# Optimization experiments

Measured on AMD Instinct MI355X. Metric: run time of the kernel, lower is better.

The kernel has to match this reference:

```python
import jax, jax.numpy as jnp
import numpy as np
from jax import lax

SCALE = 0.05  # keep gates out of saturation

def _lstm_layer(x, w_ih, w_hh, b_ih, b_hh):
    # x: [B, T, In]; w_ih: [4H, In]; w_hh: [4H, H]; PyTorch gate order i,f,g,o
    B = x.shape[0]
    H = w_hh.shape[1]
    # precompute input contribution for all timesteps: [B, T, 4H]
    xg = jnp.einsum('bti,gi->btg', x, w_ih) + b_ih + b_hh
    h0 = jnp.zeros((B, H), dtype=x.dtype)
    c0 = jnp.zeros((B, H), dtype=x.dtype)

    def step(carry, xg_t):
        h, c = carry
        gates = xg_t + h @ w_hh.T  # [B, 4H]
        i, f, g, o = jnp.split(gates, 4, axis=-1)
        i = jax.nn.sigmoid(i)
        f = jax.nn.sigmoid(f)
        g = jnp.tanh(g)
        o = jax.nn.sigmoid(o)
        c = f * c + i * g
        h = o * jnp.tanh(c)
        return (h, c), h

    (h_T, c_T), hs = lax.scan(step, (h0, c0), xg.transpose(1, 0, 2))  # hs: [T, B, H]
    return hs.transpose(1, 0, 2), h_T, c_T


def setup_inputs() -> dict:
    key = jax.random.key(0)
    ks = jax.random.split(key, 12)
    B, T, In, H = 128, 1024, 128, 256
    G = 4 * H
    inp = {
        'x': jax.random.normal(ks[0], (B, T, In), dtype=jnp.float32),
        'w_ih_l0': jax.random.normal(ks[1], (G, In), dtype=jnp.float32) * SCALE,
        'w_hh_l0': jax.random.normal(ks[2], (G, H), dtype=jnp.float32) * SCALE,
        'b_ih_l0': jax.random.normal(ks[3], (G,), dtype=jnp.float32) * SCALE,
        'b_hh_l0': jax.random.normal(ks[4], (G,), dtype=jnp.float32) * SCALE,
        'w_ih_l1': jax.random.normal(ks[5], (G, H), dtype=jnp.float32) * SCALE,
        'w_hh_l1': jax.random.normal(ks[6], (G, H), dtype=jnp.float32) * SCALE,
        'b_ih_l1': jax.random.normal(ks[7], (G,), dtype=jnp.float32) * SCALE,
        'b_hh_l1': jax.random.normal(ks[8], (G,), dtype=jnp.float32) * SCALE,
        'w_lin': jax.random.normal(ks[9], (In, H), dtype=jnp.float32) * SCALE,
        'b_lin': jax.random.normal(ks[10], (In,), dtype=jnp.float32) * SCALE,
    }
    return inp


def reference(x, w_ih_l0, w_hh_l0, b_ih_l0, b_hh_l0,
              w_ih_l1, w_hh_l1, b_ih_l1, b_hh_l1, w_lin, b_lin):
    h0_seq, h0, c0 = _lstm_layer(x, w_ih_l0, w_hh_l0, b_ih_l0, b_hh_l0)
    h1_seq, h1, c1 = _lstm_layer(h0_seq, w_ih_l1, w_hh_l1, b_ih_l1, b_hh_l1)
    out = jnp.einsum('bth,oh->bto', h1_seq, w_lin) + b_lin  # [B, T, In]
    h = jnp.stack([h0, h1], axis=0)  # [num_layers, B, H]
    c = jnp.stack([c0, c1], axis=0)
    return out, (h, c)
```

## Files before the change

### kernel.cpp

```cpp
#include <hip/hip_runtime.h>
#include <hip/hip_bf16.h>

typedef __attribute__((ext_vector_type(8))) short short8;
typedef __attribute__((ext_vector_type(4))) float floatx4;
typedef __attribute__((ext_vector_type(4))) unsigned int uint4v;
typedef __attribute__((ext_vector_type(2))) _Float16 f16x2;

#define B_ 128
#define T_ 1024
#define H_ 256
#define G_ 1024

#if defined(__has_builtin)
#  if __has_builtin(__builtin_amdgcn_fdot2)
#    define HAS_FDOT2 1
#  endif
#endif

__device__ __forceinline__ float sigmoidf_(float x) {
    x = fminf(fmaxf(x, -30.f), 30.f);
    return 1.0f / (1.0f + __expf(-x));
}
__device__ __forceinline__ float tanhf_(float x) {
    x = fminf(fmaxf(x, -15.f), 15.f);
    float e = __expf(2.0f * x);
    return 1.0f - 2.0f / (e + 1.0f);
}
__device__ __forceinline__ unsigned short f2bu(float x) {
    __hip_bfloat16 b = __float2bfloat16(x);
    return *reinterpret_cast<unsigned short*>(&b);
}

__device__ __forceinline__ float dot2_(unsigned int w, unsigned int h, float acc) {
#ifdef HAS_FDOT2
    return __builtin_amdgcn_fdot2(__builtin_bit_cast(f16x2, w),
                                  __builtin_bit_cast(f16x2, h), acc, false);
#else
    float d;
    asm("v_dot2_f32_f16 %0, %1, %2, %3" : "=v"(d) : "v"(w), "v"(h), "v"(acc));
    return d;
#endif
}

__global__ __launch_bounds__(256) void gemm_bias_f32(
    const float* __restrict__ A,
    const float* __restrict__ Wt,
    const float* __restrict__ bias1,
    const float* __restrict__ bias2,
    float* __restrict__ C,
    int d2shift, long sa1, long sa2, long sc1, long sc2, int K)
{
    __shared__ __hip_bfloat16 a_tile[64][40];
    __shared__ __hip_bfloat16 b_tile[64][40];

    const int tid  = threadIdx.x;
    const int wave = tid >> 6;
    const int lane = tid & 63;
    const int quad = lane >> 4;
    const int l16  = lane & 15;

    const int bm = blockIdx.x * 64;
    const int bn = blockIdx.y * 64;
    const int mask = (1 << d2shift) - 1;

    const int lr  = tid >> 2;
    const int seg = tid & 3;

    const int grow = bm + lr;
    const float* abase =
        A + (long)(grow >> d2shift) * sa1 + (long)(grow & mask) * sa2 + seg * 8;
    const float* bbase = Wt + (long)(bn + lr) * K + seg * 8;

    floatx4 acc[4];
    #pragma unroll
    for (int nt = 0; nt < 4; ++nt) acc[nt] = (floatx4){0.f, 0.f, 0.f, 0.f};

    for (int kk = 0; kk < K; kk += 32) {
        float4 a0 = *(const float4*)(abase + kk);
        float4 a1 = *(const float4*)(abase + kk + 4);
        float4 b0 = *(const float4*)(bbase + kk);
        float4 b1 = *(const float4*)(bbase + kk + 4);
        uint4 ap, bp;
        ap.x = f2bu(a0.x) | ((unsigned)f2bu(a0.y) << 16);
        ap.y = f2bu(a0.z) | ((unsigned)f2bu(a0.w) << 16);
        ap.z = f2bu(a1.x) | ((unsigned)f2bu(a1.y) << 16);
        ap.w = f2bu(a1.z) | ((unsigned)f2bu(a1.w) << 16);
        bp.x = f2bu(b0.x) | ((unsigned)f2bu(b0.y) << 16);
        bp.y = f2bu(b0.z) | ((unsigned)f2bu(b0.w) << 16);
        bp.z = f2bu(b1.x) | ((unsigned)f2bu(b1.y) << 16);
        bp.w = f2bu(b1.z) | ((unsigned)f2bu(b1.w) << 16);
        __syncthreads();
        *(uint4*)&a_tile[lr][seg * 8] = ap;
        *(uint4*)&b_tile[lr][seg * 8] = bp;
        __syncthreads();
        short8 af = *(const short8*)&a_tile[wave * 16 + l16][quad * 8];
        #pragma unroll
        for (int nt = 0; nt < 4; ++nt) {
            short8 bf = *(const short8*)&b_tile[nt * 16 + l16][quad * 8];
            acc[nt] = __builtin_amdgcn_mfma_f32_16x16x32_bf16(af, bf, acc[nt], 0, 0, 0);
        }
    }

    #pragma unroll
    for (int nt = 0; nt < 4; ++nt) {
        const int col = bn + nt * 16 + l16;
        float bsum = bias1[col];
        if (bias2) bsum += bias2[col];
        #pragma unroll
        for (int r = 0; r < 4; ++r) {
            const int rm = bm + wave * 16 + quad * 4 + r;
            const long off = (long)(rm >> d2shift) * sc1 + (long)(rm & mask) * sc2;
            C[off + col] = acc[nt][r] + bsum;
        }
    }
}

__global__ __launch_bounds__(256) void pack_whh(
    const float* __restrict__ w,
    unsigned int* __restrict__ wrg,
    unsigned int* __restrict__ wo)
{
    const int idx = blockIdx.x * 256 + threadIdx.x;
    if (idx < 98304) {
        const int kh = idx / 49152;
        const int r  = idx % 49152;
        const int g  = r >> 14;
        const int r2 = r & 16383;
        const int kp = r2 >> 8;
        const int jj = r2 & 255;
        const long src = (long)(g * 256 + jj) * 256 + kh * 128 + kp * 2;
        f16x2 pk;
        pk.x = (_Float16)w[src];
        pk.y = (_Float16)w[src + 1];
        wrg[idx] = __builtin_bit_cast(unsigned int, pk);
    } else {
        const int i2 = idx - 98304;
        const int jj = i2 >> 7;
        const int kp = i2 & 127;
        const long src = (long)(768 + jj) * 256 + kp * 2;
        f16x2 pk;
        pk.x = (_Float16)w[src];
        pk.y = (_Float16)w[src + 1];
        wo[i2] = __builtin_bit_cast(unsigned int, pk);
    }
}

struct LArgs {
    const float* xg;
    const unsigned int* wrg;
    const unsigned int* wo;
    float* h_seq;
    const float* h_in;
    const float* c_in;
    float* h_out;
    float* c_out;
    float* c_fin;
    int Tc;
    int init;
    int valid;
};

__device__ __forceinline__ void lstm_body(const LArgs& A, int b)
{
    const int tid = threadIdx.x;
    const int j   = tid & 255;
    const int kh  = tid >> 8;

    __shared__ __align__(16) unsigned int wo_lds[32768];
    __shared__ __align__(16) float part[256][4];
    __shared__ __align__(16) _Float16 hpk[256];

    const int Tc = A.Tc;

    unsigned int wi_[64], wf_[64], wg_[64];
    {
        const unsigned int* wb = A.wrg + (long)kh * 49152 + j;
        #pragma unroll
        for (int kp = 0; kp < 64; ++kp) wi_[kp] = wb[kp * 256];
        #pragma unroll
        for (int kp = 0; kp < 64; ++kp) wf_[kp] = wb[16384 + kp * 256];
        #pragma unroll
        for (int kp = 0; kp < 64; ++kp) wg_[kp] = wb[32768 + kp * 256];
    }

    for (int it = 0; it < 64; ++it) {
        const int d    = it * 512 + tid;
        const int jr   = d >> 7;
        const int kp   = d & 127;
        const int slot = (kp >> 2) ^ (jr & 31);
        wo_lds[jr * 128 + slot * 4 + (kp & 3)] = A.wo[d];
    }

    float c = 0.f, hlast = 0.f;
    if (kh == 0) {
        float h0 = 0.f;
        if (!A.init) {
            h0 = A.h_in[(long)b * H_ + j];
            c  = A.c_in[(long)b * H_ + j];
        }
        hlast = h0;
        hpk[j] = (_Float16)h0;
    }
    __syncthreads();

    const float* xbase = A.xg + (long)b * G_ + j;
    float nI = 0.f, nF = 0.f, nG = 0.f, nO = 0.f;
    if (kh == 0) {
        nI = xbase[0]; nF = xbase[256]; nG = xbase[512]; nO = xbase[768];
    }

    const int jx = j & 31;

    for (int t = 0; t < Tc; ++t) {
        __syncthreads();

        float aI = nI, aF = nF, aG = nG, aO = nO;
        if (kh == 0 && t + 1 < Tc) {
            const float* xn = xbase + (long)(t + 1) * (B_ * G_);
            nI = xn[0]; nF = xn[256]; nG = xn[512]; nO = xn[768];
        }

        #pragma unroll
        for (int q = 0; q < 16; ++q) {
            const int gi = kh * 16 + q;
            uint4v hv = *(const uint4v*)&hpk[gi * 8];
            uint4v wv = *(const uint4v*)&wo_lds[j * 128 + ((gi ^ jx) << 2)];
            #pragma unroll
            for (int e = 0; e < 4; ++e) {
                const int kp = q * 4 + e;
                aI = dot2_(wi_[kp], hv[e], aI);
                aF = dot2_(wf_[kp], hv[e], aF);
                aG = dot2_(wg_[kp], hv[e], aG);
                aO = dot2_(wv[e],   hv[e], aO);
            }
        }

        if (kh) {
            float4 pp; pp.x = aI; pp.y = aF; pp.z = aG; pp.w = aO;
            *(float4*)&part[j][0] = pp;
        }
        __syncthreads();
        if (!kh) {
            float4 pp = *(const float4*)&part[j][0];
            const float iv = sigmoidf_(aI + pp.x);
            const float fv = sigmoidf_(aF + pp.y);
            const float gv = tanhf_(aG + pp.z);
            const float ov = sigmoidf_(aO + pp.w);
            c = fv * c + iv * gv;
            const float hv2 = ov * tanhf_(c);
            hlast = hv2;
            A.h_seq[((long)t * B_ + b) * H_ + j] = hv2;
            hpk[j] = (_Float16)hv2;
        }
    }

    if (kh == 0) {
        A.h_out[(long)b * H_ + j] = hlast;
        A.c_out[(long)b * H_ + j] = c;
        if (A.c_fin) A.c_fin[(long)b * H_ + j] = c;
    }
}

__global__ __launch_bounds__(512, 2) void lstm_fused(LArgs a0, LArgs a1)
{
    const LArgs& A = (blockIdx.x < 128) ? a0 : a1;
    if (!A.valid) return;
    lstm_body(A, blockIdx.x & 127);
}

extern "C" void kernel_launch(void* const* d_in, const int* in_sizes, int n_in,
                              void* d_out, int out_size, void* d_ws, size_t ws_size,
                              hipStream_t stream)
{
    const float* x     = (const float*)d_in[0];
    const float* w_ih0 = (const float*)d_in[1];
    const float* w_hh0 = (const float*)d_in[2];
    const float* b_ih0 = (const float*)d_in[3];
    const float* b_hh0 = (const float*)d_in[4];
    const float* w_ih1 = (const float*)d_in[5];
    const float* w_hh1 = (const float*)d_in[6];
    const float* b_ih1 = (const float*)d_in[7];
    const float* b_hh1 = (const float*)d_in[8];
    const float* w_lin = (const float*)d_in[9];
    const float* b_lin = (const float*)d_in[10];

    float* out  = (float*)d_out;
    float* hfin = out + (size_t)B_ * T_ * 128;
    float* cfin = hfin + 2 * (B_ * H_);

    char* p = (char*)d_ws;
    unsigned int* wp0 = (unsigned int*)p;  p += 131072 * 4;
    unsigned int* wp1 = (unsigned int*)p;  p += 131072 * 4;
    float* h0st = (float*)p;  p += 131072;
    float* h1st = (float*)p;  p += 131072;
    float* c0st = (float*)p;  p += 131072;
    float* c1st = (float*)p;  p += 131072;
    const size_t fixed = (size_t)(p - (char*)d_ws);

    int Tc = 1024;
    while (Tc > 1 && fixed + (size_t)Tc * 1310720u > ws_size) Tc >>= 1;
    const int nc = T_ / Tc;
    const int tshift = __builtin_ctz((unsigned)Tc);

    float* xg0 = (float*)p;  p += (size_t)Tc * 524288;
    float* xg1 = (float*)p;  p += (size_t)Tc * 524288;
    float* h0c = (float*)p;  p += (size_t)Tc * 131072;
    float* h1c = (float*)p;

    pack_whh<<<dim3(512), dim3(256), 0, stream>>>(w_hh0, wp0, wp0 + 98304);
    pack_whh<<<dim3(512), dim3(256), 0, stream>>>(w_hh1, wp1, wp1 + 98304);

    LArgs inv{};  inv.valid = 0;

    auto L0args = [&](int i) {
        LArgs a;
        a.xg = xg0; a.wrg = wp0; a.wo = wp0 + 98304;
        a.h_seq = h0c; a.h_in = h0st; a.c_in = c0st;
        a.h_out = (i == nc - 1) ? hfin : h0st;
        a.c_out = c0st;
        a.c_fin = (i == nc - 1) ? cfin : (float*)nullptr;
        a.Tc = Tc; a.init = (i == 0); a.valid = 1;
        return a;
    };
    auto L1args = [&](int i) {
        LArgs a;
        a.xg = xg1; a.wrg = wp1; a.wo = wp1 + 98304;
        a.h_seq = h1c; a.h_in = h1st; a.c_in = c1st;
        a.h_out = (i == nc - 1) ? (hfin + B_ * H_) : h1st;
        a.c_out = c1st;
        a.c_fin = (i == nc - 1) ? (cfin + B_ * H_) : (float*)nullptr;
        a.Tc = Tc; a.init = (i == 0); a.valid = 1;
        return a;
    };

    auto gemm0 = [&](int i) {
        gemm_bias_f32<<<dim3(2 * Tc, 16), dim3(256), 0, stream>>>(
            x + (long)i * Tc * 128, w_ih0, b_ih0, b_hh0, xg0,
            7, 128L, 131072L, 131072L, 1024L, 128);
    };

    gemm0(0);
    lstm_fused<<<dim3(256), dim3(512), 0, stream>>>(inv, L0args(0));

    for (int i = 0; i < nc; ++i) {
        gemm_bias_f32<<<dim3(2 * Tc, 16), dim3(256), 0, stream>>>(
            h0c, w_ih1, b_ih1, b_hh1, xg1,
            7, 32768L, 256L, 131072L, 1024L, 256);

        if (i + 1 < nc) gemm0(i + 1);

        lstm_fused<<<dim3(256), dim3(512), 0, stream>>>(
            L1args(i), (i + 1 < nc) ? L0args(i + 1) : inv);

        gemm_bias_f32<<<dim3(2 * Tc, 2), dim3(256), 0, stream>>>(
            h1c, w_lin, b_lin, (const float*)nullptr, out + (long)i * Tc * 128,
            tshift, 256L, 32768L, 131072L, 128L, 256);
    }
}
```

Measured before the change: 2.400 ms.

## Split LSTM recurrence K across four lanes with DPP reduction and double-buffered h

The recurrent step now splits the hidden-state K dimension four ways across adjacent lanes (1024 threads per block) instead of two ways across wave halves. Partial sums are combined with DPP quad shuffles rather than an LDS round-trip, which removes one of the two barriers per timestep. The h vector is double-buffered in LDS. Per-thread register weights drop from 192 to 96, and all four lanes redundantly compute the gate nonlinearities. The launch bound of 1024 threads with 4 blocks may be unachievable and could spill registers, and the xg prefetch is dropped, so its load latency now sits on the serial path.

```diff
diff --git a/kernel.cpp b/kernel.cpp
--- a/kernel.cpp
+++ b/kernel.cpp
@@ -40,6 +40,15 @@
     asm("v_dot2_f32_f16 %0, %1, %2, %3" : "=v"(d) : "v"(w), "v"(h), "v"(acc));
     return d;
 #endif
+}
+
+__device__ __forceinline__ float qsum_(float x) {
+    int a = __builtin_bit_cast(int, x);
+    int b = __builtin_amdgcn_mov_dpp(a, 0xB1, 0xf, 0xf, true);
+    float s = x + __builtin_bit_cast(float, b);
+    int c = __builtin_bit_cast(int, s);
+    int d = __builtin_amdgcn_mov_dpp(c, 0x4E, 0xf, 0xf, true);
+    return s + __builtin_bit_cast(float, d);
 }
 
 __global__ __launch_bounds__(256) void gemm_bias_f32(
@@ -122,13 +131,13 @@
 {
     const int idx = blockIdx.x * 256 + threadIdx.x;
     if (idx < 98304) {
-        const int kh = idx / 49152;
-        const int r  = idx % 49152;
-        const int g  = r >> 14;
-        const int r2 = r & 16383;
+        const int kq = idx / 24576;
+        const int r  = idx % 24576;
+        const int g  = r >> 13;
+        const int r2 = r & 8191;
         const int kp = r2 >> 8;
         const int jj = r2 & 255;
-        const long src = (long)(g * 256 + jj) * 256 + kh * 128 + kp * 2;
+        const long src = (long)(g * 256 + jj) * 256 + kq * 64 + kp * 2;
         f16x2 pk;
         pk.x = (_Float16)w[src];
         pk.y = (_Float16)w[src + 1];
@@ -163,28 +172,27 @@
 __device__ __forceinline__ void lstm_body(const LArgs& A, int b)
 {
     const int tid = threadIdx.x;
-    const int j   = tid & 255;
-    const int kh  = tid >> 8;
+    const int j   = tid >> 2;
+    const int kq  = tid & 3;
 
     __shared__ __align__(16) unsigned int wo_lds[32768];
-    __shared__ __align__(16) float part[256][4];
-    __shared__ __align__(16) _Float16 hpk[256];
+    __shared__ __align__(16) _Float16 hpk[2][4][72];
 
     const int Tc = A.Tc;
 
-    unsigned int wi_[64], wf_[64], wg_[64];
+    unsigned int wi_[32], wf_[32], wg_[32];
     {
-        const unsigned int* wb = A.wrg + (long)kh * 49152 + j;
-        #pragma unroll
-        for (int kp = 0; kp < 64; ++kp) wi_[kp] = wb[kp * 256];
-        #pragma unroll
-        for (int kp = 0; kp < 64; ++kp) wf_[kp] = wb[16384 + kp * 256];
-        #pragma unroll
-        for (int kp = 0; kp < 64; ++kp) wg_[kp] = wb[32768 + kp * 256];
-    }
-
-    for (int it = 0; it < 64; ++it) {
-        const int d    = it * 512 + tid;
+        const unsigned int* wb = A.wrg + (long)kq * 24576 + j;
+        #pragma unroll
+        for (int kp = 0; kp < 32; ++kp) wi_[kp] = wb[kp * 256];
+        #pragma unroll
+        for (int kp = 0; kp < 32; ++kp) wf_[kp] = wb[8192 + kp * 256];
+        #pragma unroll
+        for (int kp = 0; kp < 32; ++kp) wg_[kp] = wb[16384 + kp * 256];
+    }
+
+    for (int it = 0; it < 32; ++it) {
+        const int d    = it * 1024 + tid;
         const int jr   = d >> 7;
         const int kp   = d & 127;
         const int slot = (kp >> 2) ^ (jr & 31);
@@ -192,39 +200,28 @@
     }
 
     float c = 0.f, hlast = 0.f;
-    if (kh == 0) {
-        float h0 = 0.f;
-        if (!A.init) {
-            h0 = A.h_in[(long)b * H_ + j];
-            c  = A.c_in[(long)b * H_ + j];
-        }
+    if (!A.init) c = A.c_in[(long)b * H_ + j];
+    if (kq == 0) {
+        float h0 = A.init ? 0.f : A.h_in[(long)b * H_ + j];
         hlast = h0;
-        hpk[j] = (_Float16)h0;
+        hpk[0][j >> 6][j & 63] = (_Float16)h0;
     }
     __syncthreads();
 
     const float* xbase = A.xg + (long)b * G_ + j;
-    float nI = 0.f, nF = 0.f, nG = 0.f, nO = 0.f;
-    if (kh == 0) {
-        nI = xbase[0]; nF = xbase[256]; nG = xbase[512]; nO = xbase[768];
-    }
-
     const int jx = j & 31;
+    const unsigned int* worow = wo_lds + j * 128;
 
     for (int t = 0; t < Tc; ++t) {
-        __syncthreads();
-
-        float aI = nI, aF = nF, aG = nG, aO = nO;
-        if (kh == 0 && t + 1 < Tc) {
-            const float* xn = xbase + (long)(t + 1) * (B_ * G_);
-            nI = xn[0]; nF = xn[256]; nG = xn[512]; nO = xn[768];
-        }
-
-        #pragma unroll
-        for (int q = 0; q < 16; ++q) {
-            const int gi = kh * 16 + q;
-            uint4v hv = *(const uint4v*)&hpk[gi * 8];
-            uint4v wv = *(const uint4v*)&wo_lds[j * 128 + ((gi ^ jx) << 2)];
+        const float* xt = xbase + (long)t * (B_ * G_);
+        const float xI = xt[0], xF = xt[256], xG = xt[512], xO = xt[768];
+
+        float aI = 0.f, aF = 0.f, aG = 0.f, aO = 0.f;
+        const _Float16* hq = &hpk[t & 1][kq][0];
+        #pragma unroll
+        for (int q = 0; q < 8; ++q) {
+            uint4v hv = *(const uint4v*)(hq + q * 8);
+            uint4v wv = *(const uint4v*)(worow + (((kq * 8 + q) ^ jx) << 2));
             #pragma unroll
             for (int e = 0; e < 4; ++e) {
                 const int kp = q * 4 + e;
@@ -235,33 +232,30 @@
             }
         }
 
-        if (kh) {
-            float4 pp; pp.x = aI; pp.y = aF; pp.z = aG; pp.w = aO;
-            *(float4*)&part[j][0] = pp;
+        aI = qsum_(aI); aF = qsum_(aF); aG = qsum_(aG); aO = qsum_(aO);
+
+        const float iv = sigmoidf_(xI + aI);
+        const float fv = sigmoidf_(xF + aF);
+        const float gv = tanhf_(xG + aG);
+        const float ov = sigmoidf_(xO + aO);
+        c = fv * c + iv * gv;
+        const float hv2 = ov * tanhf_(c);
+        hlast = hv2;
+        if (kq == 0) {
+            A.h_seq[((long)t * B_ + b) * H_ + j] = hv2;
+            hpk[(t + 1) & 1][j >> 6][j & 63] = (_Float16)hv2;
         }
         __syncthreads();
-        if (!kh) {
-            float4 pp = *(const float4*)&part[j][0];
-            const float iv = sigmoidf_(aI + pp.x);
-            const float fv = sigmoidf_(aF + pp.y);
-            const float gv = tanhf_(aG + pp.z);
-            const float ov = sigmoidf_(aO + pp.w);
-            c = fv * c + iv * gv;
-            const float hv2 = ov * tanhf_(c);
-            hlast = hv2;
-            A.h_seq[((long)t * B_ + b) * H_ + j] = hv2;
-            hpk[j] = (_Float16)hv2;
-        }
-    }
-
-    if (kh == 0) {
+    }
+
+    if (kq == 0) {
         A.h_out[(long)b * H_ + j] = hlast;
         A.c_out[(long)b * H_ + j] = c;
         if (A.c_fin) A.c_fin[(long)b * H_ + j] = c;
     }
 }
 
-__global__ __launch_bounds__(512, 2) void lstm_fused(LArgs a0, LArgs a1)
+__global__ __launch_bounds__(1024, 4) void lstm_fused(LArgs a0, LArgs a1)
 {
     const LArgs& A = (blockIdx.x < 128) ? a0 : a1;
     if (!A.valid) return;
@@ -340,7 +334,7 @@
     };
 
     gemm0(0);
-    lstm_fused<<<dim3(256), dim3(512), 0, stream>>>(inv, L0args(0));
+    lstm_fused<<<dim3(256), dim3(1024), 0, stream>>>(inv, L0args(0));
 
     for (int i = 0; i < nc; ++i) {
         gemm_bias_f32<<<dim3(2 * Tc, 16), dim3(256), 0, stream>>>(
@@ -349,7 +343,7 @@
 
         if (i + 1 < nc) gemm0(i + 1);
 
-        lstm_fused<<<dim3(256), dim3(512), 0, stream>>>(
+        lstm_fused<<<dim3(256), dim3(1024), 0, stream>>>(
             L1args(i), (i + 1 < nc) ? L0args(i + 1) : inv);
 
         gemm_bias_f32<<<dim3(2 * Tc, 2), dim3(256), 0, stream>>>(
```

After: 3.566 ms. 1.49x slower.

## Broadcast hidden state via readlane, double-buffer h, pre-swizzle W_o

Applied to the files above, without the earlier changes.

Each lane now reads one packed h pair from LDS and the recurrent dot products broadcast it across the wave with readlane, replacing per-iteration 16-byte vector LDS loads of h. The h buffer is double-buffered by timestep and the loop-top barrier moves to the loop end. The XOR swizzle of the output-gate weights moves into the host-side packing kernel, so the in-kernel LDS fill becomes a plain copy. The cost is 64 readlane instructions per step, which are scalar-pipe operations and may serialize against the dot2 stream.

```diff
diff --git a/kernel.cpp b/kernel.cpp
--- a/kernel.cpp
+++ b/kernel.cpp
@@ -137,11 +137,14 @@
         const int i2 = idx - 98304;
         const int jj = i2 >> 7;
         const int kp = i2 & 127;
+        const int g  = kp >> 2;
+        const int e  = kp & 3;
+        const int s  = (g ^ (jj & 31)) & 31;
         const long src = (long)(768 + jj) * 256 + kp * 2;
         f16x2 pk;
         pk.x = (_Float16)w[src];
         pk.y = (_Float16)w[src + 1];
-        wo[i2] = __builtin_bit_cast(unsigned int, pk);
+        wo[jj * 128 + s * 4 + e] = __builtin_bit_cast(unsigned int, pk);
     }
 }
 
@@ -162,13 +165,16 @@
 
 __device__ __forceinline__ void lstm_body(const LArgs& A, int b)
 {
-    const int tid = threadIdx.x;
-    const int j   = tid & 255;
-    const int kh  = tid >> 8;
+    const int tid  = threadIdx.x;
+    const int wv_  = tid >> 6;
+    const int lane = tid & 63;
+    const int kh   = wv_ >> 2;
+    const int j    = ((wv_ & 3) << 6) | lane;
+    const bool epi = (kh == 0);
 
     __shared__ __align__(16) unsigned int wo_lds[32768];
     __shared__ __align__(16) float part[256][4];
-    __shared__ __align__(16) _Float16 hpk[256];
+    __shared__ __align__(16) _Float16 hpk[2][256];
 
     const int Tc = A.Tc;
 
@@ -184,63 +190,62 @@
     }
 
     for (int it = 0; it < 64; ++it) {
-        const int d    = it * 512 + tid;
-        const int jr   = d >> 7;
-        const int kp   = d & 127;
-        const int slot = (kp >> 2) ^ (jr & 31);
-        wo_lds[jr * 128 + slot * 4 + (kp & 3)] = A.wo[d];
+        const int d = it * 512 + tid;
+        wo_lds[d] = A.wo[d];
     }
 
     float c = 0.f, hlast = 0.f;
-    if (kh == 0) {
+    if (epi) {
         float h0 = 0.f;
         if (!A.init) {
             h0 = A.h_in[(long)b * H_ + j];
             c  = A.c_in[(long)b * H_ + j];
         }
         hlast = h0;
-        hpk[j] = (_Float16)h0;
+        hpk[0][j] = (_Float16)h0;
     }
     __syncthreads();
 
     const float* xbase = A.xg + (long)b * G_ + j;
     float nI = 0.f, nF = 0.f, nG = 0.f, nO = 0.f;
-    if (kh == 0) {
+    if (epi) {
         nI = xbase[0]; nF = xbase[256]; nG = xbase[512]; nO = xbase[768];
     }
 
+    const unsigned int* worow = wo_lds + j * 128;
     const int jx = j & 31;
 
     for (int t = 0; t < Tc; ++t) {
-        __syncthreads();
+        const unsigned int hvec =
+            *(const unsigned int*)&hpk[t & 1][(kh << 7) + lane * 2];
 
         float aI = nI, aF = nF, aG = nG, aO = nO;
-        if (kh == 0 && t + 1 < Tc) {
+        if (epi && t + 1 < Tc) {
             const float* xn = xbase + (long)(t + 1) * (B_ * G_);
             nI = xn[0]; nF = xn[256]; nG = xn[512]; nO = xn[768];
         }
 
         #pragma unroll
         for (int q = 0; q < 16; ++q) {
-            const int gi = kh * 16 + q;
-            uint4v hv = *(const uint4v*)&hpk[gi * 8];
-            uint4v wv = *(const uint4v*)&wo_lds[j * 128 + ((gi ^ jx) << 2)];
+            uint4v wo4 = *(const uint4v*)(worow + ((((kh << 4) + q) ^ jx) << 2));
             #pragma unroll
             for (int e = 0; e < 4; ++e) {
                 const int kp = q * 4 + e;
-                aI = dot2_(wi_[kp], hv[e], aI);
-                aF = dot2_(wf_[kp], hv[e], aF);
-                aG = dot2_(wg_[kp], hv[e], aG);
-                aO = dot2_(wv[e],   hv[e], aO);
+                const unsigned int sh =
+                    (unsigned int)__builtin_amdgcn_readlane((int)hvec, kp);
+                aI = dot2_(wi_[kp], sh, aI);
+                aF = dot2_(wf_[kp], sh, aF);
+                aG = dot2_(wg_[kp], sh, aG);
+                aO = dot2_(wo4[e],  sh, aO);
             }
         }
 
-        if (kh) {
+        if (!epi) {
             float4 pp; pp.x = aI; pp.y = aF; pp.z = aG; pp.w = aO;
             *(float4*)&part[j][0] = pp;
         }
         __syncthreads();
-        if (!kh) {
+        if (epi) {
             float4 pp = *(const float4*)&part[j][0];
             const float iv = sigmoidf_(aI + pp.x);
             const float fv = sigmoidf_(aF + pp.y);
@@ -250,11 +255,12 @@
             const float hv2 = ov * tanhf_(c);
             hlast = hv2;
             A.h_seq[((long)t * B_ + b) * H_ + j] = hv2;
-            hpk[j] = (_Float16)hv2;
-        }
-    }
-
-    if (kh == 0) {
+            hpk[(t + 1) & 1][j] = (_Float16)hv2;
+        }
+        __syncthreads();
+    }
+
+    if (epi) {
         A.h_out[(long)b * H_ + j] = hlast;
         A.c_out[(long)b * H_ + j] = c;
         if (A.c_fin) A.c_fin[(long)b * H_ + j] = c;
```

Result: slower. 2.659 ms (+10.8%).

## Merge per-chunk input-projection and output GEMMs into one multi-problem launch

Applied to the files above, without the earlier changes.

Packs the layer-1 input projection, the next chunk's layer-0 input projection, and the previous chunk's output projection into a single GEMM launch whose grid y-dimension selects the sub-problem. The output projection for a chunk is deferred one iteration so it can share that launch, with a final standalone launch for the last chunk. This is meant to cut kernel launches and let the small output GEMM fill the GPU alongside the larger ones. It also drops the input clamps in sigmoid and tanh, which saves a few instructions but relies on __expf overflow behaviour being benign.

```diff
diff --git a/kernel.cpp b/kernel.cpp
--- a/kernel.cpp
+++ b/kernel.cpp
@@ -18,11 +18,9 @@
 #endif
 
 __device__ __forceinline__ float sigmoidf_(float x) {
-    x = fminf(fmaxf(x, -30.f), 30.f);
     return 1.0f / (1.0f + __expf(-x));
 }
 __device__ __forceinline__ float tanhf_(float x) {
-    x = fminf(fmaxf(x, -15.f), 15.f);
     float e = __expf(2.0f * x);
     return 1.0f - 2.0f / (e + 1.0f);
 }
@@ -42,13 +40,19 @@
 #endif
 }
 
-__global__ __launch_bounds__(256) void gemm_bias_f32(
-    const float* __restrict__ A,
-    const float* __restrict__ Wt,
-    const float* __restrict__ bias1,
-    const float* __restrict__ bias2,
-    float* __restrict__ C,
-    int d2shift, long sa1, long sa2, long sc1, long sc2, int K)
+struct GParam {
+    const float* A;
+    const float* Wt;
+    const float* bias1;
+    const float* bias2;
+    float* C;
+    int d2shift;
+    long sa1, sa2, sc1, sc2;
+    int K;
+    int valid;
+};
+
+__device__ __forceinline__ void gemm_core(const GParam& P, int bm, int bn)
 {
     __shared__ __hip_bfloat16 a_tile[64][40];
     __shared__ __hip_bfloat16 b_tile[64][40];
@@ -59,23 +63,21 @@
     const int quad = lane >> 4;
     const int l16  = lane & 15;
 
-    const int bm = blockIdx.x * 64;
-    const int bn = blockIdx.y * 64;
-    const int mask = (1 << d2shift) - 1;
+    const int mask = (1 << P.d2shift) - 1;
 
     const int lr  = tid >> 2;
     const int seg = tid & 3;
 
     const int grow = bm + lr;
     const float* abase =
-        A + (long)(grow >> d2shift) * sa1 + (long)(grow & mask) * sa2 + seg * 8;
-    const float* bbase = Wt + (long)(bn + lr) * K + seg * 8;
+        P.A + (long)(grow >> P.d2shift) * P.sa1 + (long)(grow & mask) * P.sa2 + seg * 8;
+    const float* bbase = P.Wt + (long)(bn + lr) * P.K + seg * 8;
 
     floatx4 acc[4];
     #pragma unroll
     for (int nt = 0; nt < 4; ++nt) acc[nt] = (floatx4){0.f, 0.f, 0.f, 0.f};
 
-    for (int kk = 0; kk < K; kk += 32) {
+    for (int kk = 0; kk < P.K; kk += 32) {
         float4 a0 = *(const float4*)(abase + kk);
         float4 a1 = *(const float4*)(abase + kk + 4);
         float4 b0 = *(const float4*)(bbase + kk);
@@ -104,15 +106,29 @@
     #pragma unroll
     for (int nt = 0; nt < 4; ++nt) {
         const int col = bn + nt * 16 + l16;
-        float bsum = bias1[col];
-        if (bias2) bsum += bias2[col];
+        float bsum = P.bias1[col];
+        if (P.bias2) bsum += P.bias2[col];
         #pragma unroll
         for (int r = 0; r < 4; ++r) {
             const int rm = bm + wave * 16 + quad * 4 + r;
-            const long off = (long)(rm >> d2shift) * sc1 + (long)(rm & mask) * sc2;
-            C[off + col] = acc[nt][r] + bsum;
-        }
-    }
+            const long off = (long)(rm >> P.d2shift) * P.sc1 + (long)(rm & mask) * P.sc2;
+            P.C[off + col] = acc[nt][r] + bsum;
+        }
+    }
+}
+
+__global__ __launch_bounds__(256) void gemm_bias_f32(GParam P)
+{
+    gemm_core(P, blockIdx.x * 64, blockIdx.y * 64);
+}
+
+__global__ __launch_bounds__(256) void gemm_mega(GParam p0, GParam p1, GParam p2)
+{
+    const int y = blockIdx.y;
+    const GParam& P = (y < 16) ? p0 : (y < 32 ? p1 : p2);
+    if (!P.valid) return;
+    const int ln = (y < 16) ? y : (y < 32 ? y - 16 : y - 32);
+    gemm_core(P, blockIdx.x * 64, ln * 64);
 }
 
 __global__ __launch_bounds__(256) void pack_whh(
@@ -311,6 +327,7 @@
     pack_whh<<<dim3(512), dim3(256), 0, stream>>>(w_hh1, wp1, wp1 + 98304);
 
     LArgs inv{};  inv.valid = 0;
+    GParam ginv{}; ginv.valid = 0;
 
     auto L0args = [&](int i) {
         LArgs a;
@@ -333,27 +350,43 @@
         return a;
     };
 
-    auto gemm0 = [&](int i) {
-        gemm_bias_f32<<<dim3(2 * Tc, 16), dim3(256), 0, stream>>>(
-            x + (long)i * Tc * 128, w_ih0, b_ih0, b_hh0, xg0,
-            7, 128L, 131072L, 131072L, 1024L, 128);
-    };
-
-    gemm0(0);
+    auto Pg0 = [&](int i) {
+        GParam P;
+        P.A = x + (long)i * Tc * 128; P.Wt = w_ih0; P.bias1 = b_ih0; P.bias2 = b_hh0;
+        P.C = xg0; P.d2shift = 7;
+        P.sa1 = 128L; P.sa2 = 131072L; P.sc1 = 131072L; P.sc2 = 1024L;
+        P.K = 128; P.valid = 1;
+        return P;
+    };
+    auto Pg1 = [&](int i) {
+        GParam P;
+        P.A = h0c; P.Wt = w_ih1; P.bias1 = b_ih1; P.bias2 = b_hh1;
+        P.C = xg1; P.d2shift = 7;
+        P.sa1 = 32768L; P.sa2 = 256L; P.sc1 = 131072L; P.sc2 = 1024L;
+        P.K = 256; P.valid = 1;
+        return P;
+    };
+    auto Pout = [&](int i) {
+        GParam P;
+        P.A = h1c; P.Wt = w_lin; P.bias1 = b_lin; P.bias2 = nullptr;
+        P.C = out + (long)i * Tc * 128; P.d2shift = tshift;
+        P.sa1 = 256L; P.sa2 = 32768L; P.sc1 = 131072L; P.sc2 = 128L;
+        P.K = 256; P.valid = 1;
+        return P;
+    };
+
+    gemm_bias_f32<<<dim3(2 * Tc, 16), dim3(256), 0, stream>>>(Pg0(0));
     lstm_fused<<<dim3(256), dim3(512), 0, stream>>>(inv, L0args(0));
 
     for (int i = 0; i < nc; ++i) {
-        gemm_bias_f32<<<dim3(2 * Tc, 16), dim3(256), 0, stream>>>(
-            h0c, w_ih1, b_ih1, b_hh1, xg1,
-            7, 32768L, 256L, 131072L, 1024L, 256);
-
-        if (i + 1 < nc) gemm0(i + 1);
+        gemm_mega<<<dim3(2 * Tc, 34), dim3(256), 0, stream>>>(
+            Pg1(i),
+            (i + 1 < nc) ? Pg0(i + 1) : ginv,
+            (i > 0) ? Pout(i - 1) : ginv);
 
         lstm_fused<<<dim3(256), dim3(512), 0, stream>>>(
             L1args(i), (i + 1 < nc) ? L0args(i + 1) : inv);
-
-        gemm_bias_f32<<<dim3(2 * Tc, 2), dim3(256), 0, stream>>>(
-            h1c, w_lin, b_lin, (const float*)nullptr, out + (long)i * Tc * 128,
-            tshift, 256L, 32768L, 131072L, 128L, 256);
-    }
-}
+    }
+
+    gemm_bias_f32<<<dim3(2 * Tc, 2), dim3(256), 0, stream>>>(Pout(nc - 1));
+}
```

Measured after the change: 2.607 ms. +8.7%, slower.
